# Kernel tuning notes

Measured on AMD Instinct MI355X. Metric: run time of the kernel, lower is better.

The kernel has to match this reference:

```python
import jax, jax.numpy as jnp
import numpy as np

TWO_PI = 2.0 * np.pi


def _unwrap(x):
    # torch: abs(x - 2*pi*round(x/(2*pi))) -> wrap to principal value, take magnitude
    return jnp.abs(x - TWO_PI * jnp.round(x / TWO_PI))


def _shift_diff_last(x):
    # Equivalent to matmul with M = triu(1,d=1)-triu(1,d=2)-eye (superdiag=+1, diag=-1):
    # out[..., 0] = -x[..., 0]; out[..., j] = x[..., j-1] - x[..., j]
    return jnp.concatenate([-x[..., :1], x[..., :-1] - x[..., 1:]], axis=-1)


def setup_inputs() -> dict:
    key = jax.random.key(0)
    k1, k2, k3, k4 = jax.random.split(key, 4)
    shape = (32, 1, 513, 512)  # [B, 1, nfreqs, frames]
    return {
        "spec_est_real": jax.random.normal(k1, shape, dtype=jnp.float32),
        "spec_est_imag": jax.random.normal(k2, shape, dtype=jnp.float32),
        "spec_ref_real": jax.random.normal(k3, shape, dtype=jnp.float32),
        "spec_ref_imag": jax.random.normal(k4, shape, dtype=jnp.float32),
    }


def reference(spec_est_real, spec_est_imag, spec_ref_real, spec_ref_imag):
    # torch.angle(complex).squeeze(1) -> [B, F, T]
    phase_g = jnp.arctan2(spec_est_imag, spec_est_real)[:, 0]
    phase_r = jnp.arctan2(spec_ref_imag, spec_ref_real)[:, 0]

    d = phase_r - phase_g  # [B, F, T]

    # IP loss
    ip_loss = jnp.mean(_unwrap(d))
    # GD: shift-difference along freq axis (GD_r - GD_g = shift_diff(phase_r - phase_g))
    gd_loss = jnp.mean(_unwrap(_shift_diff_last(jnp.swapaxes(d, 1, 2))))
    # PTD: shift-difference along time axis
    ptd_loss = jnp.mean(_unwrap(_shift_diff_last(d)))

    return ip_loss + gd_loss + ptd_loss
```

## Files before the change

### kernel.cpp

```cpp
#include <hip/hip_runtime.h>
#include <math.h>


#define NB 32
#define NF 513
#define NT 512
#define BPC 32
#define CHUNKS 17
#define NBLOCKS 544
#define NTOT 8404992LL

static __device__ __forceinline__ float fast_atan2(float y, float x) {
    const float PI_F  = 3.14159274101257324f;
    const float PI_2F = 1.57079632679489662f;
    float ax = fabsf(x), ay = fabsf(y);
    float mx = fmaxf(ax, ay), mn = fminf(ax, ay);
    float r  = mn * __builtin_amdgcn_rcpf(mx);
    r = (mx == 0.f) ? 0.f : r;
    float s = r * r;
    float p = fmaf(s, -0.01172120f, 0.05265332f);
    p = fmaf(s, p, -0.11643287f);
    p = fmaf(s, p,  0.19354346f);
    p = fmaf(s, p, -0.33262347f);
    p = fmaf(s, p,  0.99997726f);
    float a = r * p;
    a = (ay > ax) ? (PI_2F - a) : a;
    a = (x < 0.f) ? (PI_F - a) : a;
    return copysignf(a, y);
}

static __device__ __forceinline__ float pdiff(float a, float b, float c, float d) {
    return fast_atan2(fmaf(d, a, -(c * b)), fmaf(c, a, d * b));
}

static __device__ __forceinline__ float wrap_abs(float x) {
    const float PI_F     = 3.14159274101257324f;
    const float TWO_PI_F = 6.28318548202514648f;
    float u = fabsf(x);
    return u > PI_F ? TWO_PI_F - u : u;
}

struct Row8 { float4 a0, a1, b0, b1, c0, c1, e0, e1; };

static __device__ __forceinline__ void calc8(const Row8& r, float d[8]) {
    d[0] = pdiff(r.a0.x, r.b0.x, r.c0.x, r.e0.x);
    d[1] = pdiff(r.a0.y, r.b0.y, r.c0.y, r.e0.y);
    d[2] = pdiff(r.a0.z, r.b0.z, r.c0.z, r.e0.z);
    d[3] = pdiff(r.a0.w, r.b0.w, r.c0.w, r.e0.w);
    d[4] = pdiff(r.a1.x, r.b1.x, r.c1.x, r.e1.x);
    d[5] = pdiff(r.a1.y, r.b1.y, r.c1.y, r.e1.y);
    d[6] = pdiff(r.a1.z, r.b1.z, r.c1.z, r.e1.z);
    d[7] = pdiff(r.a1.w, r.b1.w, r.c1.w, r.e1.w);
}

static __device__ __forceinline__ float acc_row(const float d[8], float dp[8], int lane) {
    float dt = __shfl_up(d[7], 1, 64);
    if (lane == 0) dt = 0.f;
    float s = 0.f;
    #pragma unroll
    for (int k = 0; k < 8; ++k) {
        s += fabsf(d[k]);
        s += wrap_abs(dp[k] - d[k]);
        s += wrap_abs(dt - d[k]);
        dt = d[k];
        dp[k] = d[k];
    }
    return s;
}

__global__ __launch_bounds__(256) void phase_loss_k(
    const float* __restrict__ er, const float* __restrict__ ei,
    const float* __restrict__ rr, const float* __restrict__ ri,
    float* __restrict__ slots)
{
    __shared__ float halo[4][NT];
    __shared__ float ws4[4];
    const int tid  = threadIdx.x;
    const int lane = tid & 63;
    const int wave = tid >> 6;
    const int wid  = blockIdx.x;
    const int b    = wid / CHUNKS;
    const int f0b  = (wid - b * CHUNKS) * BPC;
    const int f0w  = f0b + wave * 8;
    const int base = b * (NF * NT);
    const int rem  = NF - f0w;
    const int nv   = rem < 8 ? (rem < 0 ? 0 : rem) : 8;

#define LOAD_ROW(dst, f_) do {                                   \
        const int _i = base + (f_) * NT + lane * 8;              \
        dst.a0 = *(const float4*)(er + _i);                      \
        dst.a1 = *(const float4*)(er + _i + 4);                  \
        dst.b0 = *(const float4*)(ei + _i);                      \
        dst.b1 = *(const float4*)(ei + _i + 4);                  \
        dst.c0 = *(const float4*)(rr + _i);                      \
        dst.c1 = *(const float4*)(rr + _i + 4);                  \
        dst.e0 = *(const float4*)(ri + _i);                      \
        dst.e1 = *(const float4*)(ri + _i + 4);                  \
    } while (0)

    Row8 R7, Rh;
    const bool full  = (nv == 8);
    const bool whalo = (wave == 0) && (f0b > 0) && (nv > 0);
    if (full)  LOAD_ROW(R7, f0w + 7);
    if (whalo) LOAD_ROW(Rh, f0b - 1);

    float d7[8];
    if (full) {
        calc8(R7, d7);
        if (wave < 3) {
            *(float4*)&halo[wave + 1][lane * 8]     = make_float4(d7[0], d7[1], d7[2], d7[3]);
            *(float4*)&halo[wave + 1][lane * 8 + 4] = make_float4(d7[4], d7[5], d7[6], d7[7]);
        }
    }
    if (whalo) {
        float dh[8];
        calc8(Rh, dh);
        *(float4*)&halo[0][lane * 8]     = make_float4(dh[0], dh[1], dh[2], dh[3]);
        *(float4*)&halo[0][lane * 8 + 4] = make_float4(dh[4], dh[5], dh[6], dh[7]);
    }
    __syncthreads();

    float s = 0.f;
    if (nv > 0) {
        float dp[8];
        if (f0w > 0) {
            float4 h0 = *(const float4*)&halo[wave][lane * 8];
            float4 h1 = *(const float4*)&halo[wave][lane * 8 + 4];
            dp[0] = h0.x; dp[1] = h0.y; dp[2] = h0.z; dp[3] = h0.w;
            dp[4] = h1.x; dp[5] = h1.y; dp[6] = h1.z; dp[7] = h1.w;
        } else {
            #pragma unroll
            for (int k = 0; k < 8; ++k) dp[k] = 0.f;
        }

        const int nfresh = full ? 7 : nv;
        Row8 cur, nxt;
        LOAD_ROW(nxt, f0w);
        #pragma unroll
        for (int r = 0; r < 7; ++r) {
            if (r >= nfresh) break;
            cur = nxt;
            if (r + 1 < nfresh) LOAD_ROW(nxt, f0w + r + 1);
            float d[8];
            calc8(cur, d);
            s += acc_row(d, dp, lane);
        }
        if (full) s += acc_row(d7, dp, lane);
    }
#undef LOAD_ROW

    #pragma unroll
    for (int off = 32; off > 0; off >>= 1)
        s += __shfl_down(s, off, 64);
    if (lane == 0) ws4[wave] = s;
    __syncthreads();
    if (tid == 0) slots[blockIdx.x] = ws4[0] + ws4[1] + ws4[2] + ws4[3];
}

__global__ __launch_bounds__(256) void finalize_k(const float* __restrict__ slots,
                                                  float* __restrict__ out)
{
    int tid = threadIdx.x;
    float s = 0.f;
    for (int i = tid; i < NBLOCKS; i += 256) s += slots[i];
    #pragma unroll
    for (int off = 32; off > 0; off >>= 1)
        s += __shfl_down(s, off, 64);
    __shared__ float wsum[4];
    if ((tid & 63) == 0) wsum[tid >> 6] = s;
    __syncthreads();
    if (tid == 0) {
        double tot = (double)wsum[0] + (double)wsum[1] + (double)wsum[2] + (double)wsum[3];
        out[0] = (float)(tot / (double)NTOT);
    }
}

extern "C" void kernel_launch(void* const* d_in, const int* in_sizes, int n_in,
                              void* d_out, int out_size, void* d_ws, size_t ws_size,
                              hipStream_t stream) {
    const float* er = (const float*)d_in[0];
    const float* ei = (const float*)d_in[1];
    const float* rr = (const float*)d_in[2];
    const float* ri = (const float*)d_in[3];
    float* out   = (float*)d_out;
    float* slots = (float*)d_ws;

    phase_loss_k<<<NBLOCKS, 256, 0, stream>>>(er, ei, rr, ri, slots);
    finalize_k<<<1, 256, 0, stream>>>(slots, out);
}
```

Measured before the change: 33.89 us.

## Flatten batch-frequency rows to balance work across blocks without idle tail waves

Treats all batch and frequency rows as one flat sequence of 16416 rows, split over 512 blocks of 32 or 33 rows, instead of 17 chunks per batch where the last chunk holds a single row. This removes the mostly idle blocks and waves at each batch's frequency edge and evens out per-block load on the GPU. The price is per-row modulo tracking to reset the frequency-difference state at batch boundaries, a loop that is no longer fully unrolled, and a variable last wave.

```diff
diff --git a/kernel.cpp b/kernel.cpp
--- a/kernel.cpp
+++ b/kernel.cpp
@@ -5,9 +5,8 @@
 #define NB 32
 #define NF 513
 #define NT 512
-#define BPC 32
-#define CHUNKS 17
-#define NBLOCKS 544
+#define NROWS 16416
+#define NBLOCKS 512
 #define NTOT 8404992LL
 
 static __device__ __forceinline__ float fast_atan2(float y, float x) {
@@ -78,16 +77,17 @@
     const int tid  = threadIdx.x;
     const int lane = tid & 63;
     const int wave = tid >> 6;
-    const int wid  = blockIdx.x;
-    const int b    = wid / CHUNKS;
-    const int f0b  = (wid - b * CHUNKS) * BPC;
-    const int f0w  = f0b + wave * 8;
-    const int base = b * (NF * NT);
-    const int rem  = NF - f0w;
-    const int nv   = rem < 8 ? (rem < 0 ? 0 : rem) : 8;
+    const int bid  = blockIdx.x;
 
-#define LOAD_ROW(dst, f_) do {                                   \
-        const int _i = base + (f_) * NT + lane * 8;              \
+    int R0, N;
+    if (bid < 480) { R0 = bid * 32;                  N = 32; }
+    else           { R0 = 15360 + (bid - 480) * 33;  N = 33; }
+    const int r0w = R0 + wave * 8;
+    const int nw  = (wave == 3) ? (N - 24) : 8;
+    const int fw  = r0w % NF;
+
+#define LOAD_ROWR(dst, row_) do {                                \
+        const int _i = (row_) * NT + lane * 8;                   \
         dst.a0 = *(const float4*)(er + _i);                      \
         dst.a1 = *(const float4*)(er + _i + 4);                  \
         dst.b0 = *(const float4*)(ei + _i);                      \
@@ -99,18 +99,15 @@
     } while (0)
 
     Row8 R7, Rh;
-    const bool full  = (nv == 8);
-    const bool whalo = (wave == 0) && (f0b > 0) && (nv > 0);
-    if (full)  LOAD_ROW(R7, f0w + 7);
-    if (whalo) LOAD_ROW(Rh, f0b - 1);
-
     float d7[8];
-    if (full) {
+    const bool haveSeed = (wave < 3);
+    const bool whalo    = (wave == 0) && (fw != 0);
+    if (haveSeed) LOAD_ROWR(R7, r0w + 7);
+    if (whalo)    LOAD_ROWR(Rh, r0w - 1);
+    if (haveSeed) {
         calc8(R7, d7);
-        if (wave < 3) {
-            *(float4*)&halo[wave + 1][lane * 8]     = make_float4(d7[0], d7[1], d7[2], d7[3]);
-            *(float4*)&halo[wave + 1][lane * 8 + 4] = make_float4(d7[4], d7[5], d7[6], d7[7]);
-        }
+        *(float4*)&halo[wave + 1][lane * 8]     = make_float4(d7[0], d7[1], d7[2], d7[3]);
+        *(float4*)&halo[wave + 1][lane * 8 + 4] = make_float4(d7[4], d7[5], d7[6], d7[7]);
     }
     if (whalo) {
         float dh[8];
@@ -120,41 +117,49 @@
     }
     __syncthreads();
 
+    float dp[8];
+    if (fw != 0) {
+        float4 h0 = *(const float4*)&halo[wave][lane * 8];
+        float4 h1 = *(const float4*)&halo[wave][lane * 8 + 4];
+        dp[0] = h0.x; dp[1] = h0.y; dp[2] = h0.z; dp[3] = h0.w;
+        dp[4] = h1.x; dp[5] = h1.y; dp[6] = h1.z; dp[7] = h1.w;
+    } else {
+        #pragma unroll
+        for (int k = 0; k < 8; ++k) dp[k] = 0.f;
+    }
+
     float s = 0.f;
-    if (nv > 0) {
-        float dp[8];
-        if (f0w > 0) {
-            float4 h0 = *(const float4*)&halo[wave][lane * 8];
-            float4 h1 = *(const float4*)&halo[wave][lane * 8 + 4];
-            dp[0] = h0.x; dp[1] = h0.y; dp[2] = h0.z; dp[3] = h0.w;
-            dp[4] = h1.x; dp[5] = h1.y; dp[6] = h1.z; dp[7] = h1.w;
-        } else {
+    const int nfresh = haveSeed ? 7 : nw;
+    int f = fw;
+    Row8 cur, nxt;
+    LOAD_ROWR(nxt, r0w);
+    for (int i = 0; i < nfresh; ++i) {
+        cur = nxt;
+        if (i + 1 < nfresh) LOAD_ROWR(nxt, r0w + i + 1);
+        float d[8];
+        calc8(cur, d);
+        if (f == 0) {
             #pragma unroll
             for (int k = 0; k < 8; ++k) dp[k] = 0.f;
         }
-
-        const int nfresh = full ? 7 : nv;
-        Row8 cur, nxt;
-        LOAD_ROW(nxt, f0w);
-        #pragma unroll
-        for (int r = 0; r < 7; ++r) {
-            if (r >= nfresh) break;
-            cur = nxt;
-            if (r + 1 < nfresh) LOAD_ROW(nxt, f0w + r + 1);
-            float d[8];
-            calc8(cur, d);
-            s += acc_row(d, dp, lane);
+        s += acc_row(d, dp, lane);
+        if (++f == NF) f = 0;
+    }
+    if (haveSeed) {
+        if (f == 0) {
+            #pragma unroll
+            for (int k = 0; k < 8; ++k) dp[k] = 0.f;
         }
-        if (full) s += acc_row(d7, dp, lane);
+        s += acc_row(d7, dp, lane);
     }
-#undef LOAD_ROW
+#undef LOAD_ROWR
 
     #pragma unroll
     for (int off = 32; off > 0; off >>= 1)
         s += __shfl_down(s, off, 64);
     if (lane == 0) ws4[wave] = s;
     __syncthreads();
-    if (tid == 0) slots[blockIdx.x] = ws4[0] + ws4[1] + ws4[2] + ws4[3];
+    if (tid == 0) slots[bid] = ws4[0] + ws4[1] + ws4[2] + ws4[3];
 }
 
 __global__ __launch_bounds__(256) void finalize_k(const float* __restrict__ slots,
```

Measured after the change: 32.33 us. 1.05x faster.
